# Kernel optimization log

Hardware: AMD Instinct MI355X
Metric: run time of the kernel (lower is better)

Reference implementation:

```python
import jax, jax.numpy as jnp
import numpy as np

N = 50000; E = 320000; DIN = 768; D = 256; R = 4; L = 3
B = 64; T = 6; SD = 128; SH = 256; NC = 14; ALPHA = 0.15
NEG = -1e30


def setup_inputs():
    keys = iter(jax.random.split(jax.random.key(0), 64))
    def nrm(shape, s=0.02):
        return s * jax.random.normal(next(keys), shape, dtype=jnp.float32)
    inp = {}
    inp["x"] = jax.random.normal(next(keys), (N, DIN), dtype=jnp.float32)
    inp["edge_index"] = jax.random.randint(next(keys), (2, E), 0, N)
    inp["edge_type"] = jax.random.randint(next(keys), (E,), 0, R)
    inp["batch"] = jnp.sort(jax.random.randint(next(keys), (N,), 0, B))
    inp["sequence"] = jax.random.normal(next(keys), (B, T, SD), dtype=jnp.float32)
    inp["proj_W"] = nrm((D, DIN)); inp["proj_b"] = nrm((D,))
    inp["Wr"] = nrm((L, R, D, D))
    inp["Ws"] = nrm((L, D, D)); inp["bs"] = nrm((L, D))
    inp["att_W1"] = nrm((L, R, D // 2, 2 * D)); inp["att_b1"] = nrm((L, R, D // 2))
    inp["att_W2"] = nrm((L, R, D // 2)); inp["att_b2"] = nrm((L, R))
    inp["emb"] = nrm((L, R, D // 4), 0.1)
    inp["imp"] = jnp.tile(jnp.array([1.2, 1.1, 1.4, 0.9], dtype=jnp.float32), (L, 1))
    inp["ln_g"] = jnp.ones((L, D), jnp.float32); inp["ln_b"] = jnp.zeros((L, D), jnp.float32)
    inp["gm_W1"] = nrm((D // 2, D)); inp["gm_b1"] = nrm((D // 2,))
    inp["gm_W2"] = nrm((D // 4, D // 2)); inp["gm_b2"] = nrm((D // 4,))
    inp["gm_W3"] = nrm((NC, D // 4)); inp["gm_b3"] = nrm((NC,))
    inp["gru_Wih"] = nrm((2, 3 * SH, SD)); inp["gru_Whh"] = nrm((2, 3 * SH, SH))
    inp["gru_bih"] = nrm((2, 3 * SH)); inp["gru_bhh"] = nrm((2, 3 * SH))
    inp["sm_W1"] = nrm((SH, 2 * SH)); inp["sm_b1"] = nrm((SH,))
    inp["sm_W2"] = nrm((SH // 2, SH)); inp["sm_b2"] = nrm((SH // 2,))
    inp["sm_W3"] = nrm((NC, SH // 2)); inp["sm_b3"] = nrm((NC,))
    return inp


def _gru_dir(x, Wih, Whh, bih, bhh):  # x: [B,T,SD] -> [B,T,SH], torch GRU equations
    def step(h, xt):
        gi = xt @ Wih.T + bih
        gh = h @ Whh.T + bhh
        ir, iz, in_ = jnp.split(gi, 3, axis=-1)
        hr, hz, hn = jnp.split(gh, 3, axis=-1)
        r = jax.nn.sigmoid(ir + hr)
        z = jax.nn.sigmoid(iz + hz)
        n = jnp.tanh(in_ + r * hn)
        h = (1.0 - z) * n + z * h
        return h, h
    h0 = jnp.zeros((x.shape[0], Whh.shape[1]), x.dtype)
    _, ys = jax.lax.scan(step, h0, jnp.swapaxes(x, 0, 1))
    return jnp.swapaxes(ys, 0, 1)


def _gnn_layer(h, h0, src, dst, et, Wr, Ws, bs, aW1, ab1, aW2, ab2, emb, imp, g, b):
    ew = jax.nn.softmax(imp)  # layer_edge_importance softmax over R types
    cat = jnp.concatenate([h[dst], h[src]], axis=1)  # [E, 2D] = [x_i, x_j]
    agg = jnp.zeros_like(h)
    for r in range(R):
        tx = h @ Wr[r].T  # [N, D] per-type transform
        s = jax.nn.relu(cat @ aW1[r].T + ab1[r]) @ aW2[r] + ab2[r]  # [E]
        s = jax.nn.leaky_relu(s, 0.2) + jnp.mean(emb[r])
        mask = et == r
        a = jax.nn.softmax(jnp.where(mask, s, NEG))  # softmax over all type-r edges (dim=0 in torch)
        a = jnp.where(mask, a, 0.0)
        msg = jax.ops.segment_sum(a[:, None] * tx[src], dst, num_segments=h.shape[0])
        agg = agg + ew[r] * msg
    out = (1.0 - ALPHA) * agg + h @ Ws.T + bs + ALPHA * h0
    mu = jnp.mean(out, axis=-1, keepdims=True)
    var = jnp.var(out, axis=-1, keepdims=True)
    out = (out - mu) / jnp.sqrt(var + 1e-5) * g + b  # LayerNorm (eps=1e-5)
    return jax.nn.gelu(out, approximate=False)


def _forward(x, sequence, proj_W, proj_b, Wr, Ws, bs, att_W1, att_b1, att_W2, att_b2, emb, imp, ln_g, ln_b, gm_W1, gm_b1, gm_W2, gm_b2, gm_W3, gm_b3, gru_Wih, gru_Whh, gru_bih, gru_bhh, sm_W1, sm_b1, sm_W2, sm_b2, sm_W3, sm_b3, edge_index, edge_type, batch):
    # sequence branch: bidirectional GRU, avg+max pool over time, MLP readout
    fwd = _gru_dir(sequence, gru_Wih[0], gru_Whh[0], gru_bih[0], gru_bhh[0])
    bwd = _gru_dir(sequence[:, ::-1], gru_Wih[1], gru_Whh[1], gru_bih[1], gru_bhh[1])[:, ::-1]
    seq_out = jnp.concatenate([fwd, bwd], axis=-1)  # [B, T, 2*SH]
    z = jnp.mean(seq_out, axis=1) + jnp.max(seq_out, axis=1)
    z = jax.nn.relu(z @ sm_W1.T + sm_b1)
    z = jax.nn.relu(z @ sm_W2.T + sm_b2)
    seq_logits = z @ sm_W3.T + sm_b3
    # graph branch
    src, dst = edge_index[0], edge_index[1]
    h = x @ proj_W.T + proj_b
    h0 = h
    for i in range(L):
        h = _gnn_layer(h, h0, src, dst, edge_type, Wr[i], Ws[i], bs[i], att_W1[i], att_b1[i], att_W2[i], att_b2[i], emb[i], imp[i], ln_g[i], ln_b[i])
    sums = jax.ops.segment_sum(h, batch, num_segments=B)
    cnt = jax.ops.segment_sum(jnp.ones((h.shape[0],), h.dtype), batch, num_segments=B)
    pooled = sums / jnp.clip(cnt, 1.0)[:, None]  # global_mean_pool
    gz = jax.nn.relu(pooled @ gm_W1.T + gm_b1)
    gz = jax.nn.relu(gz @ gm_W2.T + gm_b2)
    graph_logits = gz @ gm_W3.T + gm_b3
    return graph_logits + seq_logits


def reference(x, edge_index, edge_type, batch, sequence, proj_W, proj_b, Wr, Ws, bs, att_W1, att_b1, att_W2, att_b2, emb, imp, ln_g, ln_b, gm_W1, gm_b1, gm_W2, gm_b2, gm_W3, gm_b3, gru_Wih, gru_Whh, gru_bih, gru_bhh, sm_W1, sm_b1, sm_W2, sm_b2, sm_W3, sm_b3):
    return _forward(x, sequence, proj_W, proj_b, Wr, Ws, bs, att_W1, att_b1, att_W2, att_b2, emb, imp, ln_g, ln_b, gm_W1, gm_b1, gm_W2, gm_b2, gm_W3, gm_b3, gru_Wih, gru_Whh, gru_bih, gru_bhh, sm_W1, sm_b1, sm_W2, sm_b2, sm_W3, sm_b3, edge_index, edge_type, batch)
```

## Files before the change

kernel.cpp:

```cpp
#include <hip/hip_runtime.h>
#include <math.h>

#define N_NODES 50000
#define E_EDGES 320000
#define DIN_    768
#define D_      256
#define R_TYPES 4
#define L_LAYERS 3
#define BATCH_  64
#define T_STEPS 6
#define SD_     128
#define SH_     256
#define NC_     14
#define ALPHA_  0.15f
#define NBLK_B  1250
#define POOL_CHUNK 256
#define E_PAD   (E_EDGES + 256)
#define SCAN_BLK 49
#define NCAT    (D_ + R_TYPES * D_)

typedef __bf16 bf16_t;
typedef bf16_t bf16x8_t __attribute__((ext_vector_type(8)));
typedef bf16_t bf16x4_t __attribute__((ext_vector_type(4)));
typedef float  f32x4_t  __attribute__((ext_vector_type(4)));

__device__ __forceinline__ f32x4_t mfma16(bf16x8_t a, bf16x8_t b, f32x4_t c) {
    return __builtin_amdgcn_mfma_f32_16x16x32_bf16(a, b, c, 0, 0, 0);
}

__global__ void f2b_kernel(const float* __restrict__ src, bf16_t* __restrict__ dst, int n4)
{
    for (int i = blockIdx.x * blockDim.x + threadIdx.x; i < n4; i += gridDim.x * blockDim.x) {
        float4 v = ((const float4*)src)[i];
        bf16_t o[4] = {(bf16_t)v.x, (bf16_t)v.y, (bf16_t)v.z, (bf16_t)v.w};
        *(ulong1*)&dst[i * 4] = *(ulong1*)o;
    }
}

__global__ void pack_wcat_kernel(const float* __restrict__ Ws, const float* __restrict__ Wr,
                                 bf16_t* __restrict__ Wcat)
{
    int total = L_LAYERS * NCAT * D_;
    for (int i = blockIdx.x * blockDim.x + threadIdx.x; i < total; i += gridDim.x * blockDim.x) {
        int l = i / (NCAT * D_);
        int rem = i - l * NCAT * D_;
        int row = rem / D_, k = rem - row * D_;
        float v = (row < D_) ? Ws[((size_t)l * D_ + row) * D_ + k]
                             : Wr[((size_t)l * R_TYPES * D_ + (row - D_)) * D_ + k];
        Wcat[i] = (bf16_t)v;
    }
}

__global__ void transpose2_kernel(const float* __restrict__ in, float* __restrict__ out, int R, int C)
{
    int total = 2 * R * C;
    for (int i = blockIdx.x * blockDim.x + threadIdx.x; i < total; i += gridDim.x * blockDim.x) {
        int dir = i / (R * C);
        int rem = i - dir * R * C;
        int r = rem / C, c = rem - r * C;
        out[dir * R * C + c * R + r] = in[i];
    }
}

__global__ __launch_bounds__(256) void proj_mfma3(
    const bf16_t* __restrict__ A, const bf16_t* __restrict__ W,
    const float* __restrict__ bias, float* __restrict__ outf,
    bf16_t* __restrict__ outb, int M)
{
    __shared__ bf16_t As[64][44];
    __shared__ bf16_t Bs[64][44];
    const int m0 = blockIdx.x * 64;
    const int n0 = blockIdx.y * 64;
    const int tid = threadIdx.x;
    const int wave = tid >> 6, lane = tid & 63;
    const int wy = wave >> 1, wx = wave & 1;
    const int q = lane >> 4, c = lane & 15;
    const int srow = tid >> 2, skq = tid & 3;

    f32x4_t acc[2][2] = {};
    for (int k0 = 0; k0 < DIN_; k0 += 32) {
        {
            int m = m0 + srow;
            bf16x8_t av = {};
            if (m < M) av = *(const bf16x8_t*)&A[(size_t)m * DIN_ + k0 + skq * 8];
            *(bf16x8_t*)&As[srow][skq * 8] = av;
            *(bf16x8_t*)&Bs[srow][skq * 8] = *(const bf16x8_t*)&W[(size_t)(n0 + srow) * DIN_ + k0 + skq * 8];
        }
        __syncthreads();
        bf16x8_t af[2], bfv[2];
        #pragma unroll
        for (int mt = 0; mt < 2; mt++) af[mt] = *(const bf16x8_t*)&As[wy * 32 + mt * 16 + c][q * 8];
        #pragma unroll
        for (int nt = 0; nt < 2; nt++) bfv[nt] = *(const bf16x8_t*)&Bs[wx * 32 + nt * 16 + c][q * 8];
        #pragma unroll
        for (int mt = 0; mt < 2; mt++)
            #pragma unroll
            for (int nt = 0; nt < 2; nt++)
                acc[mt][nt] = mfma16(af[mt], bfv[nt], acc[mt][nt]);
        __syncthreads();
    }
    #pragma unroll
    for (int mt = 0; mt < 2; mt++) {
        #pragma unroll
        for (int nt = 0; nt < 2; nt++) {
            int n = n0 + wx * 32 + nt * 16 + c;
            float bv = bias[n];
            #pragma unroll
            for (int j = 0; j < 4; j++) {
                int m = m0 + wy * 32 + mt * 16 + q * 4 + j;
                if (m < M) {
                    float v = acc[mt][nt][j] + bv;
                    outf[(size_t)m * D_ + n] = v;
                    outb[(size_t)m * D_ + n] = (bf16_t)v;
                }
            }
        }
    }
}

__global__ __launch_bounds__(256) void linear_dual_mfma(
    const bf16_t* __restrict__ A, const bf16_t* __restrict__ W,
    const float* __restrict__ bias, float* __restrict__ outf,
    bf16_t* __restrict__ outb, int M)
{
    __shared__ bf16_t As[64][44];
    __shared__ bf16_t Bs[64][44];
    const int m0 = blockIdx.x * 64;
    const int n0 = blockIdx.y * 64;
    const int tid = threadIdx.x;
    const int wave = tid >> 6, lane = tid & 63;
    const int wy = wave >> 1, wx = wave & 1;
    const int q = lane >> 4, c = lane & 15;
    const int srow = tid >> 2, skq = tid & 3;

    f32x4_t acc[2][2] = {};
    for (int k0 = 0; k0 < D_; k0 += 32) {
        {
            int m = m0 + srow;
            bf16x8_t av = {};
            if (m < M) av = *(const bf16x8_t*)&A[(size_t)m * D_ + k0 + skq * 8];
            *(bf16x8_t*)&As[srow][skq * 8] = av;
            *(bf16x8_t*)&Bs[srow][skq * 8] = *(const bf16x8_t*)&W[(size_t)(n0 + srow) * D_ + k0 + skq * 8];
        }
        __syncthreads();
        bf16x8_t af[2], bfv[2];
        #pragma unroll
        for (int mt = 0; mt < 2; mt++) af[mt] = *(const bf16x8_t*)&As[wy * 32 + mt * 16 + c][q * 8];
        #pragma unroll
        for (int nt = 0; nt < 2; nt++) bfv[nt] = *(const bf16x8_t*)&Bs[wx * 32 + nt * 16 + c][q * 8];
        #pragma unroll
        for (int mt = 0; mt < 2; mt++)
            #pragma unroll
            for (int nt = 0; nt < 2; nt++)
                acc[mt][nt] = mfma16(af[mt], bfv[nt], acc[mt][nt]);
        __syncthreads();
    }
    #pragma unroll
    for (int mt = 0; mt < 2; mt++) {
        #pragma unroll
        for (int nt = 0; nt < 2; nt++) {
            int n = n0 + wx * 32 + nt * 16 + c;
            float bv = (n < D_) ? bias[n] : 0.0f;
            #pragma unroll
            for (int j = 0; j < 4; j++) {
                int m = m0 + wy * 32 + mt * 16 + q * 4 + j;
                if (m < M) {
                    float v = acc[mt][nt][j] + bv;
                    if (n < D_) outf[(size_t)m * D_ + n] = v;
                    else        outb[(size_t)m * (R_TYPES * D_) + (n - D_)] = (bf16_t)v;
                }
            }
        }
    }
}

__global__ __launch_bounds__(256) void bucket_count2(const int* __restrict__ et,
                                                     int* __restrict__ blockCnt)
{
    int b = blockIdx.x, tid = threadIdx.x;
    int r = et[b * 256 + tid];
    int lane = tid & 63, wv = tid >> 6;
    __shared__ int wcnt[4][4];
    #pragma unroll
    for (int t = 0; t < 4; t++) {
        unsigned long long m = __ballot(r == t);
        if (lane == 0) wcnt[wv][t] = __popcll(m);
    }
    __syncthreads();
    if (tid < 4)
        blockCnt[b * 4 + tid] = wcnt[0][tid] + wcnt[1][tid] + wcnt[2][tid] + wcnt[3][tid];
}

__global__ void bucket_scan(const int* __restrict__ blockCnt, int* __restrict__ boffP,
                            int* __restrict__ cnt, int* __restrict__ basePerBlock,
                            int* __restrict__ bsrc, int* __restrict__ bdst)
{
    __shared__ int tot[4];
    int t = threadIdx.x;
    if (t < 4) {
        int s = 0;
        for (int b = 0; b < NBLK_B; b++) s += blockCnt[b * 4 + t];
        tot[t] = s;
    }
    __syncthreads();
    if (t == 0) {
        int o = 0;
        for (int r = 0; r < 4; r++) {
            boffP[r] = o; cnt[r] = tot[r];
            o += (tot[r] + 63) & ~63;
        }
        boffP[4] = o;
    }
    __syncthreads();
    if (t < 4) {
        int run = boffP[t];
        for (int b = 0; b < NBLK_B; b++) { basePerBlock[b * 4 + t] = run; run += blockCnt[b * 4 + t]; }
    }
    __syncthreads();
    for (int r = 0; r < 4; r++) {
        int s = boffP[r] + cnt[r], e = boffP[r + 1];
        for (int i = s + t; i < e; i += 64) { bsrc[i] = 0; bdst[i] = 0; }
    }
}

__global__ __launch_bounds__(256) void bucket_scatter2(
    const int* __restrict__ ei, const int* __restrict__ et,
    const int* __restrict__ basePerBlock, int* __restrict__ bsrc, int* __restrict__ bdst)
{
    int b = blockIdx.x, tid = threadIdx.x;
    int e = b * 256 + tid;
    int r = et[e];
    int lane = tid & 63, wv = tid >> 6;
    __shared__ int wcnt[4][4];
    int myrank = 0;
    unsigned long long ltmask = (1ull << lane) - 1ull;
    #pragma unroll
    for (int t = 0; t < 4; t++) {
        unsigned long long m = __ballot(r == t);
        if (r == t) myrank = __popcll(m & ltmask);
        if (lane == 0) wcnt[wv][t] = __popcll(m);
    }
    __syncthreads();
    int wbase = 0;
    for (int w = 0; w < wv; w++) wbase += wcnt[w][r];
    int pos = basePerBlock[b * 4 + r] + wbase + myrank;
    bsrc[pos] = ei[e];
    bdst[pos] = ei[E_EDGES + e];
}

__global__ void embmean_kernel(const float* __restrict__ emb, float* __restrict__ em)
{
    int lr = threadIdx.x;
    if (lr < L_LAYERS * R_TYPES) {
        float s = 0.0f;
        for (int k = 0; k < 64; k++) s += emb[lr * 64 + k];
        em[lr] = s / 64.0f;
    }
}

__global__ __launch_bounds__(256) void deg_count_kernel(
    const int* __restrict__ bdst, const int* __restrict__ boffP, const int* __restrict__ cnt,
    int* __restrict__ deg)
{
    __shared__ int sb[5], sc[4];
    if (threadIdx.x < 5) sb[threadIdx.x] = boffP[threadIdx.x];
    if (threadIdx.x < 4) sc[threadIdx.x] = cnt[threadIdx.x];
    __syncthreads();
    int total = sb[4];
    for (int p = blockIdx.x * blockDim.x + threadIdx.x; p < total; p += gridDim.x * blockDim.x) {
        int r = 0; while (r < 3 && p >= sb[r + 1]) r++;
        if (p - sb[r] < sc[r]) atomicAdd(&deg[bdst[p]], 1);
    }
}

__global__ __launch_bounds__(256) void scan1_kernel(const int* __restrict__ deg,
                                                    int* __restrict__ rowptr, int* __restrict__ blockSum)
{
    __shared__ int sdata[256];
    int b = blockIdx.x, t = threadIdx.x;
    int idx0 = b * 1024 + t * 4;
    int d[4];
    #pragma unroll
    for (int j = 0; j < 4; j++) d[j] = (idx0 + j < N_NODES) ? deg[idx0 + j] : 0;
    int tsum = d[0] + d[1] + d[2] + d[3];
    sdata[t] = tsum;
    __syncthreads();
    for (int off = 1; off < 256; off <<= 1) {
        int v = (t >= off) ? sdata[t - off] : 0;
        __syncthreads();
        sdata[t] += v;
        __syncthreads();
    }
    int ex = sdata[t] - tsum;
    int acc = ex;
    #pragma unroll
    for (int j = 0; j < 4; j++) {
        if (idx0 + j < N_NODES) rowptr[idx0 + j] = acc;
        acc += d[j];
    }
    if (t == 255) blockSum[b] = sdata[255];
}

__global__ void scan2_kernel(const int* __restrict__ blockSum, int* __restrict__ blockOff)
{
    if (threadIdx.x == 0) {
        int o = 0;
        for (int b = 0; b < SCAN_BLK; b++) { blockOff[b] = o; o += blockSum[b]; }
    }
}

__global__ __launch_bounds__(256) void scan3_kernel(int* __restrict__ rowptr,
                                                    const int* __restrict__ blockOff,
                                                    int* __restrict__ cursor)
{
    int idx = blockIdx.x * blockDim.x + threadIdx.x;
    if (idx < N_NODES) {
        int v = rowptr[idx] + blockOff[idx >> 10];
        rowptr[idx] = v; cursor[idx] = v;
    }
    if (idx == 0) rowptr[N_NODES] = E_EDGES;
}

__global__ __launch_bounds__(256) void csr_scatter_kernel(
    const int* __restrict__ bsrc, const int* __restrict__ bdst,
    const int* __restrict__ boffP, const int* __restrict__ cnt,
    int* __restrict__ cursor, int* __restrict__ csrSrc, int* __restrict__ csrPos)
{
    __shared__ int sb[5], sc[4];
    if (threadIdx.x < 5) sb[threadIdx.x] = boffP[threadIdx.x];
    if (threadIdx.x < 4) sc[threadIdx.x] = cnt[threadIdx.x];
    __syncthreads();
    int total = sb[4];
    for (int p = blockIdx.x * blockDim.x + threadIdx.x; p < total; p += gridDim.x * blockDim.x) {
        int r = 0; while (r < 3 && p >= sb[r + 1]) r++;
        if (p - sb[r] < sc[r]) {
            int pos = atomicAdd(&cursor[bdst[p]], 1);
            csrSrc[pos] = bsrc[p];
            csrPos[pos] = p;
        }
    }
}

__global__ __launch_bounds__(256) void attn_mfma(
    const bf16_t* __restrict__ hb, const int* __restrict__ bsrc, const int* __restrict__ bdst,
    const int* __restrict__ boffP, const int* __restrict__ cnt, int l,
    const bf16_t* __restrict__ W1base, const float* __restrict__ b1base,
    const float* __restrict__ W2base, const float* __restrict__ b2base,
    const float* __restrict__ em, float* __restrict__ sbuf)
{
    const int p0 = blockIdx.x * 64;
    if (p0 >= boffP[4]) return;
    int r = 0;
    while (r < 3 && p0 >= boffP[r + 1]) r++;
    const int lr = l * R_TYPES + r;
    const int base = boffP[r];
    const int cnt_r = cnt[r];
    const bf16_t* W1 = W1base + (size_t)lr * 128 * 512;
    const float*  b1 = b1base + lr * 128;
    const float*  W2 = W2base + lr * 128;

    __shared__ int nd_d[64], nd_s[64];
    __shared__ bf16_t Acat[64][44];
    __shared__ bf16_t Bs[128][44];
    const int tid = threadIdx.x;
    if (tid < 64) nd_d[tid] = bdst[p0 + tid];
    else if (tid < 128) nd_s[tid - 64] = bsrc[p0 + tid - 64];
    __syncthreads();
    const int wave = tid >> 6, lane = tid & 63;
    const int q = lane >> 4, c = lane & 15;
    const int srow = tid >> 2, skq = tid & 3;

    f32x4_t acc[8] = {};
    for (int ks = 0; ks < 16; ks++) {
        {
            int node = (ks < 8) ? nd_d[srow] : nd_s[srow];
            int koffm = (ks & 7) * 32 + skq * 8;
            *(bf16x8_t*)&Acat[srow][skq * 8] = *(const bf16x8_t*)&hb[(size_t)node * D_ + koffm];
            #pragma unroll
            for (int s = 0; s < 2; s++) {
                int slot = tid + s * 256;
                int nrow = slot >> 2, nkq = slot & 3;
                *(bf16x8_t*)&Bs[nrow][nkq * 8] = *(const bf16x8_t*)&W1[(size_t)nrow * 512 + ks * 32 + nkq * 8];
            }
        }
        __syncthreads();
        bf16x8_t af = *(const bf16x8_t*)&Acat[wave * 16 + c][q * 8];
        #pragma unroll
        for (int nt = 0; nt < 8; nt++) {
            bf16x8_t bfv = *(const bf16x8_t*)&Bs[nt * 16 + c][q * 8];
            acc[nt] = mfma16(af, bfv, acc[nt]);
        }
        __syncthreads();
    }
    float part[4] = {0, 0, 0, 0};
    #pragma unroll
    for (int nt = 0; nt < 8; nt++) {
        int n = nt * 16 + c;
        float b1v = b1[n], w2v = W2[n];
        #pragma unroll
        for (int j = 0; j < 4; j++) {
            float v = acc[nt][j] + b1v;
            v = v > 0.0f ? v : 0.0f;
            part[j] += v * w2v;
        }
    }
    #pragma unroll
    for (int j = 0; j < 4; j++) {
        #pragma unroll
        for (int mask = 1; mask <= 8; mask <<= 1)
            part[j] += __shfl_xor(part[j], mask);
    }
    if (c == 0) {
        float b2v = b2base[lr], emv = em[lr];
        #pragma unroll
        for (int j = 0; j < 4; j++) {
            int p = p0 + wave * 16 + q * 4 + j;
            bool valid = (p - base) < cnt_r;
            float sv = part[j] + b2v;
            sv = sv > 0.0f ? sv : 0.2f * sv;
            sbuf[p] = valid ? (sv + emv) : -1e30f;
        }
    }
}

__device__ __forceinline__ unsigned fkey(float f) {
    unsigned u = __float_as_uint(f);
    return (u & 0x80000000u) ? ~u : (u | 0x80000000u);
}
__device__ __forceinline__ float fkey_inv(unsigned k) {
    unsigned u = (k & 0x80000000u) ? (k ^ 0x80000000u) : ~k;
    return __uint_as_float(u);
}

__global__ void bucket_max_kernel(const float* __restrict__ sbuf, const int* __restrict__ boffP,
                                  unsigned* __restrict__ redl)
{
    int r = blockIdx.y;
    int lo = boffP[r], hi = boffP[r + 1];
    float m = -1e30f;
    for (int i = lo + blockIdx.x * blockDim.x + threadIdx.x; i < hi; i += gridDim.x * blockDim.x)
        m = fmaxf(m, sbuf[i]);
    for (int o = 32; o; o >>= 1) m = fmaxf(m, __shfl_down(m, o));
    __shared__ float wm[4];
    int lane = threadIdx.x & 63, wv = threadIdx.x >> 6;
    if (lane == 0) wm[wv] = m;
    __syncthreads();
    if (threadIdx.x == 0) {
        float b = fmaxf(fmaxf(wm[0], wm[1]), fmaxf(wm[2], wm[3]));
        atomicMax(&redl[r * 2], fkey(b));
    }
}

__global__ void bucket_sum_kernel(const float* __restrict__ sbuf, const int* __restrict__ boffP,
                                  unsigned* __restrict__ redl)
{
    int r = blockIdx.y;
    int lo = boffP[r], hi = boffP[r + 1];
    float mxf = fkey_inv(redl[r * 2]);
    float s = 0.0f;
    for (int i = lo + blockIdx.x * blockDim.x + threadIdx.x; i < hi; i += gridDim.x * blockDim.x)
        s += expf(sbuf[i] - mxf);
    for (int o = 32; o; o >>= 1) s += __shfl_down(s, o);
    __shared__ float wm[4];
    int lane = threadIdx.x & 63, wv = threadIdx.x >> 6;
    if (lane == 0) wm[wv] = s;
    __syncthreads();
    if (threadIdx.x == 0) atomicAdd((float*)&redl[r * 2 + 1], wm[0] + wm[1] + wm[2] + wm[3]);
}

__global__ __launch_bounds__(256) void msg_ln_gelu_kernel(
    const float* __restrict__ sbuf, const bf16_t* __restrict__ txAll,
    const int* __restrict__ csrSrc, const int* __restrict__ csrPos,
    const int* __restrict__ rowptr, const int* __restrict__ boffP,
    const unsigned* __restrict__ redl, const float* __restrict__ imp, int l,
    const float* __restrict__ accb, const float* __restrict__ h0,
    const float* __restrict__ g, const float* __restrict__ bvec,
    bf16_t* __restrict__ hb)
{
    __shared__ float smx[4], sinv[4], scoef[4];
    __shared__ int sb[5];
    if (threadIdx.x == 0) {
        float e0 = expf(imp[l * 4 + 0]), e1 = expf(imp[l * 4 + 1]);
        float e2 = expf(imp[l * 4 + 2]), e3 = expf(imp[l * 4 + 3]);
        float den = e0 + e1 + e2 + e3;
        float ews[4] = {e0 / den, e1 / den, e2 / den, e3 / den};
        for (int r = 0; r < 4; r++) {
            smx[r] = fkey_inv(redl[r * 2]);
            sinv[r] = 1.0f / ((const float*)redl)[r * 2 + 1];
            scoef[r] = (1.0f - ALPHA_) * ews[r];
        }
        for (int r = 0; r <= 4; r++) sb[r] = boffP[r];
    }
    __syncthreads();
    int n = blockIdx.x * 4 + (threadIdx.x >> 6);
    if (n >= N_NODES) return;
    int lane = threadIdx.x & 63;
    int c4 = lane * 4;
    float msg[4] = {0, 0, 0, 0};
    int i0 = rowptr[n], i1 = rowptr[n + 1];
    for (int i = i0; i < i1; i++) {
        int src = csrSrc[i];
        int p = csrPos[i];
        int r = 0; while (r < 3 && p >= sb[r + 1]) r++;
        float a = expf(sbuf[p] - smx[r]) * sinv[r] * scoef[r];
        bf16x4_t tv = *(const bf16x4_t*)&txAll[(size_t)src * (R_TYPES * D_) + r * D_ + c4];
        msg[0] += a * (float)tv[0];
        msg[1] += a * (float)tv[1];
        msg[2] += a * (float)tv[2];
        msg[3] += a * (float)tv[3];
    }
    float4 ac = *(const float4*)&accb[(size_t)n * D_ + c4];
    float4 hz = *(const float4*)&h0[(size_t)n * D_ + c4];
    float v[4];
    v[0] = msg[0] + ac.x + ALPHA_ * hz.x;
    v[1] = msg[1] + ac.y + ALPHA_ * hz.y;
    v[2] = msg[2] + ac.z + ALPHA_ * hz.z;
    v[3] = msg[3] + ac.w + ALPHA_ * hz.w;
    float sum = v[0] + v[1] + v[2] + v[3];
    #pragma unroll
    for (int o = 32; o; o >>= 1) sum += __shfl_down(sum, o);
    sum = __shfl(sum, 0);
    float mean = sum * (1.0f / 256.0f);
    float sq = 0.0f;
    #pragma unroll
    for (int j = 0; j < 4; j++) { float d = v[j] - mean; sq += d * d; }
    #pragma unroll
    for (int o = 32; o; o >>= 1) sq += __shfl_down(sq, o);
    sq = __shfl(sq, 0);
    float rstd = rsqrtf(sq * (1.0f / 256.0f) + 1e-5f);
    float4 gg = *(const float4*)&g[c4];
    float4 bb = *(const float4*)&bvec[c4];
    float ga[4] = {gg.x, gg.y, gg.z, gg.w};
    float ba[4] = {bb.x, bb.y, bb.z, bb.w};
    bf16_t outb[4];
    #pragma unroll
    for (int j = 0; j < 4; j++) {
        float x = (v[j] - mean) * rstd * ga[j] + ba[j];
        float ge = 0.5f * x * (1.0f + erff(x * 0.7071067811865475f));
        outb[j] = (bf16_t)ge;
    }
    *(bf16x4_t*)&hb[(size_t)n * D_ + c4] = *(bf16x4_t*)outb;
}

__global__ __launch_bounds__(256) void pool_seg_kernel(
    const bf16_t* __restrict__ hb, const int* __restrict__ batch,
    float* __restrict__ pooled, float* __restrict__ cntb, int Nn)
{
    int start = blockIdx.x * POOL_CHUNK;
    if (start >= Nn) return;
    int end = start + POOL_CHUNK; if (end > Nn) end = Nn;
    int c = threadIdx.x;
    __shared__ int bseg[POOL_CHUNK];
    if (start + c < Nn) bseg[c] = batch[start + c];
    __syncthreads();
    float acc = 0.0f;
    int cur = bseg[0];
    int segcnt = 0;
    for (int node = start; node < end; node++) {
        int b = bseg[node - start];
        if (b != cur) {
            atomicAdd(&pooled[cur * D_ + c], acc);
            if (c == 0) atomicAdd(&cntb[cur], (float)segcnt);
            acc = 0.0f; segcnt = 0; cur = b;
        }
        acc += (float)hb[(size_t)node * D_ + c];
        segcnt++;
    }
    atomicAdd(&pooled[cur * D_ + c], acc);
    if (c == 0) atomicAdd(&cntb[cur], (float)segcnt);
}

__global__ __launch_bounds__(256) void final_mlp_kernel(
    const float* __restrict__ pooled, const float* __restrict__ cntb,
    const float* __restrict__ W1, const float* __restrict__ b1,
    const float* __restrict__ W2, const float* __restrict__ b2,
    const float* __restrict__ W3, const float* __restrict__ b3,
    const float* __restrict__ seqlg, float* __restrict__ out)
{
    int b = blockIdx.x;
    int t = threadIdx.x;
    __shared__ float p[256];
    __shared__ float z1[128];
    __shared__ float z2[64];
    float c = cntb[b]; c = c < 1.0f ? 1.0f : c;
    p[t] = pooled[b * 256 + t] / c;
    __syncthreads();
    if (t < 128) {
        float s = b1[t];
        for (int k = 0; k < 256; k++) s += p[k] * W1[t * 256 + k];
        z1[t] = s > 0.0f ? s : 0.0f;
    }
    __syncthreads();
    if (t < 64) {
        float s = b2[t];
        for (int k = 0; k < 128; k++) s += z1[k] * W2[t * 128 + k];
        z2[t] = s > 0.0f ? s : 0.0f;
    }
    __syncthreads();
    if (t < NC_) {
        float s = b3[t];
        for (int k = 0; k < 64; k++) s += z2[k] * W3[t * 64 + k];
        out[b * NC_ + t] = s + seqlg[b * NC_ + t];
    }
}

__global__ __launch_bounds__(768) void gru_full(
    const float* __restrict__ seq, const float* __restrict__ WihT,
    const float* __restrict__ bih, const float* __restrict__ WhhT,
    const float* __restrict__ bhh, float* __restrict__ outs)
{
    int blk = blockIdx.x;
    int dir = blk >> 6, b = blk & 63;
    __shared__ float xt[T_STEPS * SD_];
    __shared__ float hs[SH_];
    __shared__ float gh[768];
    __shared__ float gg[768];
    int j = threadIdx.x;
    xt[j] = seq[(size_t)b * T_STEPS * SD_ + j];
    if (j < SH_) hs[j] = 0.0f;
    __syncthreads();
    const float* Wti = WihT + (size_t)dir * SD_ * 768;
    float av[T_STEPS] = {};
    for (int k = 0; k < SD_; k++) {
        float w = Wti[(size_t)k * 768 + j];
        #pragma unroll
        for (int t = 0; t < T_STEPS; t++) av[t] += xt[t * SD_ + k] * w;
    }
    float bihv = bih[dir * 768 + j];
    float bhhv = bhh[dir * 768 + j];
    const float* Wth = WhhT + (size_t)dir * SH_ * 768;
    for (int t = 0; t < T_STEPS; t++) {
        int tin = dir ? (T_STEPS - 1 - t) : t;
        float a = bhhv;
        for (int k = 0; k < SH_; k++)
            a += hs[k] * Wth[(size_t)k * 768 + j];
        gh[j] = a;
        gg[j] = av[tin] + bihv;
        __syncthreads();
        if (j < SH_) {
            float r = 1.0f / (1.0f + expf(-(gg[j] + gh[j])));
            float z = 1.0f / (1.0f + expf(-(gg[256 + j] + gh[256 + j])));
            float n = tanhf(gg[512 + j] + r * gh[512 + j]);
            float hn = (1.0f - z) * n + z * hs[j];
            hs[j] = hn;
            outs[(((size_t)blk) * T_STEPS + tin) * SH_ + j] = hn;
        }
        __syncthreads();
    }
}

__global__ __launch_bounds__(256) void seq_mlp_kernel(
    const float* __restrict__ outs, const float* __restrict__ W1, const float* __restrict__ b1,
    const float* __restrict__ W2, const float* __restrict__ b2,
    const float* __restrict__ W3, const float* __restrict__ b3,
    float* __restrict__ seqlg)
{
    int b = blockIdx.x;
    int t = threadIdx.x;
    __shared__ float z[512];
    __shared__ float z1[256];
    __shared__ float z2[128];
    for (int c = t; c < 512; c += 256) {
        int dir = c >> 8, cc = c & 255;
        float mean = 0.0f, mx = -1e30f;
        for (int tt = 0; tt < T_STEPS; tt++) {
            float v = outs[(((size_t)dir * 64 + b) * T_STEPS + tt) * SH_ + cc];
            mean += v; mx = fmaxf(mx, v);
        }
        z[c] = mean * (1.0f / T_STEPS) + mx;
    }
    __syncthreads();
    {
        float s = b1[t];
        for (int k = 0; k < 512; k++) s += z[k] * W1[t * 512 + k];
        z1[t] = s > 0.0f ? s : 0.0f;
    }
    __syncthreads();
    if (t < 128) {
        float s = b2[t];
        for (int k = 0; k < 256; k++) s += z1[k] * W2[t * 256 + k];
        z2[t] = s > 0.0f ? s : 0.0f;
    }
    __syncthreads();
    if (t < NC_) {
        float s = b3[t];
        for (int k = 0; k < 128; k++) s += z2[k] * W3[t * 128 + k];
        seqlg[b * NC_ + t] = s;
    }
}

extern "C" void kernel_launch(void* const* d_in, const int* in_sizes, int n_in,
                              void* d_out, int out_size, void* d_ws, size_t ws_size,
                              hipStream_t stream)
{
    const float* x      = (const float*)d_in[0];
    const int*   ei     = (const int*)d_in[1];
    const int*   et     = (const int*)d_in[2];
    const int*   batch  = (const int*)d_in[3];
    const float* seq    = (const float*)d_in[4];
    const float* proj_W = (const float*)d_in[5];
    const float* proj_b = (const float*)d_in[6];
    const float* Wr     = (const float*)d_in[7];
    const float* Ws     = (const float*)d_in[8];
    const float* bs     = (const float*)d_in[9];
    const float* aW1    = (const float*)d_in[10];
    const float* ab1    = (const float*)d_in[11];
    const float* aW2    = (const float*)d_in[12];
    const float* ab2    = (const float*)d_in[13];
    const float* emb    = (const float*)d_in[14];
    const float* imp    = (const float*)d_in[15];
    const float* ln_g   = (const float*)d_in[16];
    const float* ln_b   = (const float*)d_in[17];
    const float* gmW1   = (const float*)d_in[18];
    const float* gmb1   = (const float*)d_in[19];
    const float* gmW2   = (const float*)d_in[20];
    const float* gmb2   = (const float*)d_in[21];
    const float* gmW3   = (const float*)d_in[22];
    const float* gmb3   = (const float*)d_in[23];
    const float* gWih   = (const float*)d_in[24];
    const float* gWhh   = (const float*)d_in[25];
    const float* gbih   = (const float*)d_in[26];
    const float* gbhh   = (const float*)d_in[27];
    const float* smW1   = (const float*)d_in[28];
    const float* smb1   = (const float*)d_in[29];
    const float* smW2   = (const float*)d_in[30];
    const float* smb2   = (const float*)d_in[31];
    const float* smW3   = (const float*)d_in[32];
    const float* smb3   = (const float*)d_in[33];
    float* out = (float*)d_out;

    char* ws = (char*)d_ws;
    size_t o = 0;
    auto alloc = [&](size_t bytes) -> void* {
        void* p = ws + o;
        o += (bytes + 1023) & ~(size_t)1023;
        return p;
    };
    float*  h0     = (float*)alloc(sizeof(float) * (size_t)N_NODES * D_);
    float*  accb   = (float*)alloc(sizeof(float) * (size_t)N_NODES * D_);
    bf16_t* hbb    = (bf16_t*)alloc(sizeof(bf16_t) * (size_t)N_NODES * D_);
    bf16_t* xb     = (bf16_t*)alloc(sizeof(bf16_t) * (size_t)N_NODES * DIN_);
    bf16_t* txAll  = (bf16_t*)alloc(sizeof(bf16_t) * (size_t)N_NODES * R_TYPES * D_);
    bf16_t* projWb = (bf16_t*)alloc(sizeof(bf16_t) * D_ * DIN_);
    bf16_t* Wcat   = (bf16_t*)alloc(sizeof(bf16_t) * L_LAYERS * NCAT * D_);
    bf16_t* aW1b   = (bf16_t*)alloc(sizeof(bf16_t) * L_LAYERS * R_TYPES * 128 * 512);
    float*  sbuf   = (float*)alloc(sizeof(float) * E_PAD);
    int*    bsrc   = (int*)alloc(sizeof(int) * E_PAD);
    int*    bdst   = (int*)alloc(sizeof(int) * E_PAD);
    int*    boffP  = (int*)alloc(sizeof(int) * 8);
    int*    cnt    = (int*)alloc(sizeof(int) * 8);
    int*    blockCnt = (int*)alloc(sizeof(int) * NBLK_B * 4);
    int*    basePerBlock = (int*)alloc(sizeof(int) * NBLK_B * 4);
    int*    deg    = (int*)alloc(sizeof(int) * N_NODES);
    int*    rowptr = (int*)alloc(sizeof(int) * (N_NODES + 8));
    int*    cursor = (int*)alloc(sizeof(int) * N_NODES);
    int*    blockSum = (int*)alloc(sizeof(int) * 64);
    int*    blockOff = (int*)alloc(sizeof(int) * 64);
    int*    csrSrc = (int*)alloc(sizeof(int) * E_EDGES);
    int*    csrPos = (int*)alloc(sizeof(int) * E_EDGES);
    unsigned* red  = (unsigned*)alloc(sizeof(unsigned) * 32);
    float*  em     = (float*)alloc(sizeof(float) * 16);
    float*  seqlg  = (float*)alloc(sizeof(float) * BATCH_ * NC_);
    float*  WihT   = (float*)alloc(sizeof(float) * 2 * SD_ * 768);
    float*  WhhT   = (float*)alloc(sizeof(float) * 2 * SH_ * 768);
    float*  gruO   = (float*)alloc(sizeof(float) * 2 * BATCH_ * T_STEPS * SH_);
    float*  pooled = (float*)alloc(sizeof(float) * BATCH_ * D_);
    float*  cntb   = (float*)alloc(sizeof(float) * BATCH_);
    (void)ws_size; (void)in_sizes; (void)n_in; (void)out_size;

    hipMemsetAsync(red, 0, 32 * sizeof(unsigned), stream);
    hipMemsetAsync(pooled, 0, BATCH_ * D_ * sizeof(float), stream);
    hipMemsetAsync(cntb, 0, BATCH_ * sizeof(float), stream);
    hipMemsetAsync(deg, 0, N_NODES * sizeof(int), stream);

    f2b_kernel<<<2048, 256, 0, stream>>>(x, xb, N_NODES * DIN_ / 4);
    f2b_kernel<<<64, 256, 0, stream>>>(proj_W, projWb, D_ * DIN_ / 4);
    pack_wcat_kernel<<<512, 256, 0, stream>>>(Ws, Wr, Wcat);
    f2b_kernel<<<256, 256, 0, stream>>>(aW1, aW1b, L_LAYERS * R_TYPES * 128 * 512 / 4);
    transpose2_kernel<<<96, 256, 0, stream>>>(gWih, WihT, 768, SD_);
    transpose2_kernel<<<192, 256, 0, stream>>>(gWhh, WhhT, 768, SH_);

    bucket_count2<<<NBLK_B, 256, 0, stream>>>(et, blockCnt);
    bucket_scan<<<1, 64, 0, stream>>>(blockCnt, boffP, cnt, basePerBlock, bsrc, bdst);
    bucket_scatter2<<<NBLK_B, 256, 0, stream>>>(ei, et, basePerBlock, bsrc, bdst);
    embmean_kernel<<<1, 64, 0, stream>>>(emb, em);

    deg_count_kernel<<<1024, 256, 0, stream>>>(bdst, boffP, cnt, deg);
    scan1_kernel<<<SCAN_BLK, 256, 0, stream>>>(deg, rowptr, blockSum);
    scan2_kernel<<<1, 64, 0, stream>>>(blockSum, blockOff);
    scan3_kernel<<<(N_NODES + 255) / 256, 256, 0, stream>>>(rowptr, blockOff, cursor);
    csr_scatter_kernel<<<1024, 256, 0, stream>>>(bsrc, bdst, boffP, cnt, cursor, csrSrc, csrPos);

    gru_full<<<128, 768, 0, stream>>>(seq, WihT, gbih, WhhT, gbhh, gruO);
    seq_mlp_kernel<<<BATCH_, 256, 0, stream>>>(gruO, smW1, smb1, smW2, smb2, smW3, smb3, seqlg);

    const int MB = (N_NODES + 63) / 64;
    proj_mfma3<<<dim3(MB, D_ / 64), 256, 0, stream>>>(xb, projWb, proj_b, h0, hbb, N_NODES);
    const int ATTN_BLKS = E_PAD / 64;
    for (int l = 0; l < L_LAYERS; l++) {
        linear_dual_mfma<<<dim3(MB, NCAT / 64), 256, 0, stream>>>(
            hbb, Wcat + (size_t)l * NCAT * D_, bs + l * D_, accb, txAll, N_NODES);
        attn_mfma<<<ATTN_BLKS, 256, 0, stream>>>(hbb, bsrc, bdst, boffP, cnt, l,
                                                 aW1b, ab1, aW2, ab2, em, sbuf);
        bucket_max_kernel<<<dim3(256, 4), 256, 0, stream>>>(sbuf, boffP, red + l * 8);
        bucket_sum_kernel<<<dim3(256, 4), 256, 0, stream>>>(sbuf, boffP, red + l * 8);
        msg_ln_gelu_kernel<<<(N_NODES + 3) / 4, 256, 0, stream>>>(
            sbuf, txAll, csrSrc, csrPos, rowptr, boffP, red + l * 8, imp, l,
            accb, h0, ln_g + l * D_, ln_b + l * D_, hbb);
    }

    pool_seg_kernel<<<(N_NODES + POOL_CHUNK - 1) / POOL_CHUNK, 256, 0, stream>>>(hbb, batch, pooled, cntb, N_NODES);
    final_mlp_kernel<<<BATCH_, 256, 0, stream>>>(pooled, cntb, gmW1, gmb1, gmW2, gmb2, gmW3, gmb3, seqlg, out);
}
```

Before: 1.572 ms.

## Keep A row tile in registers and loop over all output column tiles per block

The dual linear kernel now loads each 64-row slice of the activation matrix once into registers and iterates over all 20 output column tiles inside one block, instead of launching a 2D grid that reloads A for every column tile. This cuts redundant global reads of A by the number of column tiles. In exchange the grid shrinks from MB x 20 to MB blocks, serializing work per block and raising register pressure (64 bf16x8 registers for A), which may lower occupancy and latency hiding.

```diff
diff --git a/kernel.cpp b/kernel.cpp
--- a/kernel.cpp
+++ b/kernel.cpp
@@ -118,56 +118,79 @@
     }
 }
 
-__global__ __launch_bounds__(256) void linear_dual_mfma(
+__global__ __launch_bounds__(256) void linear_dual_mfma4(
     const bf16_t* __restrict__ A, const bf16_t* __restrict__ W,
     const float* __restrict__ bias, float* __restrict__ outf,
     bf16_t* __restrict__ outb, int M)
 {
-    __shared__ bf16_t As[64][44];
-    __shared__ bf16_t Bs[64][44];
+    __shared__ bf16_t Sb[4][64][44];
     const int m0 = blockIdx.x * 64;
-    const int n0 = blockIdx.y * 64;
     const int tid = threadIdx.x;
     const int wave = tid >> 6, lane = tid & 63;
     const int wy = wave >> 1, wx = wave & 1;
     const int q = lane >> 4, c = lane & 15;
     const int srow = tid >> 2, skq = tid & 3;
 
-    f32x4_t acc[2][2] = {};
-    for (int k0 = 0; k0 < D_; k0 += 32) {
-        {
+    bf16x8_t areg[8][2];
+    #pragma unroll
+    for (int rd = 0; rd < 2; rd++) {
+        #pragma unroll
+        for (int ch = 0; ch < 4; ch++) {
+            int kc = rd * 4 + ch;
             int m = m0 + srow;
             bf16x8_t av = {};
-            if (m < M) av = *(const bf16x8_t*)&A[(size_t)m * D_ + k0 + skq * 8];
-            *(bf16x8_t*)&As[srow][skq * 8] = av;
-            *(bf16x8_t*)&Bs[srow][skq * 8] = *(const bf16x8_t*)&W[(size_t)(n0 + srow) * D_ + k0 + skq * 8];
-        }
-        __syncthreads();
-        bf16x8_t af[2], bfv[2];
-        #pragma unroll
-        for (int mt = 0; mt < 2; mt++) af[mt] = *(const bf16x8_t*)&As[wy * 32 + mt * 16 + c][q * 8];
-        #pragma unroll
-        for (int nt = 0; nt < 2; nt++) bfv[nt] = *(const bf16x8_t*)&Bs[wx * 32 + nt * 16 + c][q * 8];
-        #pragma unroll
-        for (int mt = 0; mt < 2; mt++)
+            if (m < M) av = *(const bf16x8_t*)&A[(size_t)m * D_ + kc * 32 + skq * 8];
+            *(bf16x8_t*)&Sb[ch][srow][skq * 8] = av;
+        }
+        __syncthreads();
+        #pragma unroll
+        for (int ch = 0; ch < 4; ch++)
             #pragma unroll
-            for (int nt = 0; nt < 2; nt++)
-                acc[mt][nt] = mfma16(af[mt], bfv[nt], acc[mt][nt]);
-        __syncthreads();
-    }
-    #pragma unroll
-    for (int mt = 0; mt < 2; mt++) {
-        #pragma unroll
-        for (int nt = 0; nt < 2; nt++) {
-            int n = n0 + wx * 32 + nt * 16 + c;
-            float bv = (n < D_) ? bias[n] : 0.0f;
+            for (int mt = 0; mt < 2; mt++)
+                areg[rd * 4 + ch][mt] = *(const bf16x8_t*)&Sb[ch][wy * 32 + mt * 16 + c][q * 8];
+        __syncthreads();
+    }
+
+    for (int nt = 0; nt < NCAT / 64; nt++) {
+        const int n0 = nt * 64;
+        f32x4_t acc[2][2] = {};
+        #pragma unroll
+        for (int rd = 0; rd < 2; rd++) {
             #pragma unroll
-            for (int j = 0; j < 4; j++) {
-                int m = m0 + wy * 32 + mt * 16 + q * 4 + j;
-                if (m < M) {
-                    float v = acc[mt][nt][j] + bv;
-                    if (n < D_) outf[(size_t)m * D_ + n] = v;
-                    else        outb[(size_t)m * (R_TYPES * D_) + (n - D_)] = (bf16_t)v;
+            for (int ch = 0; ch < 4; ch++) {
+                int kc = rd * 4 + ch;
+                *(bf16x8_t*)&Sb[ch][srow][skq * 8] =
+                    *(const bf16x8_t*)&W[(size_t)(n0 + srow) * D_ + kc * 32 + skq * 8];
+            }
+            __syncthreads();
+            #pragma unroll
+            for (int ch = 0; ch < 4; ch++) {
+                bf16x8_t bfv[2];
+                #pragma unroll
+                for (int nn = 0; nn < 2; nn++)
+                    bfv[nn] = *(const bf16x8_t*)&Sb[ch][wx * 32 + nn * 16 + c][q * 8];
+                #pragma unroll
+                for (int mt = 0; mt < 2; mt++)
+                    #pragma unroll
+                    for (int nn = 0; nn < 2; nn++)
+                        acc[mt][nn] = mfma16(areg[rd * 4 + ch][mt], bfv[nn], acc[mt][nn]);
+            }
+            __syncthreads();
+        }
+        #pragma unroll
+        for (int mt = 0; mt < 2; mt++) {
+            #pragma unroll
+            for (int nn = 0; nn < 2; nn++) {
+                int n = n0 + wx * 32 + nn * 16 + c;
+                float bv = (n < D_) ? bias[n] : 0.0f;
+                #pragma unroll
+                for (int j = 0; j < 4; j++) {
+                    int m = m0 + wy * 32 + mt * 16 + q * 4 + j;
+                    if (m < M) {
+                        float v = acc[mt][nn][j] + bv;
+                        if (n < D_) outf[(size_t)m * D_ + n] = v;
+                        else        outb[(size_t)m * (R_TYPES * D_) + (n - D_)] = (bf16_t)v;
+                    }
                 }
             }
         }
@@ -798,7 +821,7 @@
     proj_mfma3<<<dim3(MB, D_ / 64), 256, 0, stream>>>(xb, projWb, proj_b, h0, hbb, N_NODES);
     const int ATTN_BLKS = E_PAD / 64;
     for (int l = 0; l < L_LAYERS; l++) {
-        linear_dual_mfma<<<dim3(MB, NCAT / 64), 256, 0, stream>>>(
+        linear_dual_mfma4<<<MB, 256, 0, stream>>>(
             hbb, Wcat + (size_t)l * NCAT * D_, bs + l * D_, accb, txAll, N_NODES);
         attn_mfma<<<ATTN_BLKS, 256, 0, stream>>>(hbb, bsrc, bdst, boffP, cnt, l,
                                                  aW1b, ab1, aW2, ab2, em, sbuf);
```

New measurement: 1.592 ms. Within noise of the previous version (+1.3%).
